# Kernel optimization log

Hardware: AMD Instinct MI355X
Metric: run time of the kernel (lower is better)

## Reference

```python
import jax, jax.numpy as jnp
import numpy as np

MAX_LENGTH = 10
SOS = 0


def setup_inputs() -> dict:
    key = jax.random.key(0)
    ks = jax.random.split(key, 16)
    B, S, H, V = 64, 128, 1024, 32000
    sc = 0.02
    return {
        "encoder_outputs": jax.random.normal(ks[0], (B, S, H), jnp.float32),
        "encoder_hidden": jax.random.normal(ks[1], (1, B, H), jnp.float32),
        "target_tensor": jax.random.randint(ks[2], (B, MAX_LENGTH), 0, V),
        "embedding": jax.random.normal(ks[3], (V, H), jnp.float32) * sc,
        "Wa_w": jax.random.normal(ks[4], (H, H), jnp.float32) * sc,
        "Wa_b": jnp.zeros((H,), jnp.float32),
        "Ua_w": jax.random.normal(ks[5], (H, H), jnp.float32) * sc,
        "Ua_b": jnp.zeros((H,), jnp.float32),
        "Va_w": jax.random.normal(ks[6], (1, H), jnp.float32) * sc,
        "Va_b": jnp.zeros((1,), jnp.float32),
        "gru_wi": jax.random.normal(ks[7], (3 * H, 2 * H), jnp.float32) * sc,
        "gru_wh": jax.random.normal(ks[8], (3 * H, H), jnp.float32) * sc,
        "gru_bi": jnp.zeros((3 * H,), jnp.float32),
        "gru_bh": jnp.zeros((3 * H,), jnp.float32),
        "out_w": jax.random.normal(ks[9], (V, H), jnp.float32) * sc,
        "out_b": jnp.zeros((V,), jnp.float32),
    }


def reference(encoder_outputs, encoder_hidden, target_tensor, embedding,
              Wa_w, Wa_b, Ua_w, Ua_b, Va_w, Va_b,
              gru_wi, gru_wh, gru_bi, gru_bh, out_w, out_b):
    B, S, H = encoder_outputs.shape
    # teacher-forced input tokens: [SOS, tgt_0, ..., tgt_{T-2}]
    tokens = jnp.concatenate(
        [jnp.full((B, 1), SOS, dtype=target_tensor.dtype),
         target_tensor[:, :MAX_LENGTH - 1]], axis=1)  # [B, T]
    emb_seq = embedding[tokens]                         # [B, T, H] (dropout = identity)
    # precompute Ua(keys), shared across steps
    Ua_keys = jnp.einsum('bsh,kh->bsk', encoder_outputs, Ua_w) + Ua_b  # [B,S,H]
    va = Va_w[0]

    def step(h, emb_t):  # h: [B,H], emb_t: [B,H]
        q = h @ Wa_w.T + Wa_b                                   # [B,H]
        scores = jnp.einsum('bsh,h->bs', jnp.tanh(q[:, None, :] + Ua_keys), va) + Va_b[0]
        w = jax.nn.softmax(scores, axis=-1)                     # [B,S]
        ctx = jnp.einsum('bs,bsh->bh', w, encoder_outputs)      # [B,H]
        x = jnp.concatenate([emb_t, ctx], axis=-1)              # [B,2H]
        gi = x @ gru_wi.T + gru_bi                              # [B,3H]
        gh = h @ gru_wh.T + gru_bh
        r = jax.nn.sigmoid(gi[:, :H] + gh[:, :H])
        z = jax.nn.sigmoid(gi[:, H:2 * H] + gh[:, H:2 * H])
        n = jnp.tanh(gi[:, 2 * H:] + r * gh[:, 2 * H:])
        h_new = (1.0 - z) * n + z * h
        return h_new, (h_new, w)

    h0 = encoder_hidden[0]  # [B,H]
    h_final, (outs, attns) = jax.lax.scan(step, h0, jnp.swapaxes(emb_seq, 0, 1))
    outs = jnp.swapaxes(outs, 0, 1)                 # [B,T,H]
    attns = jnp.swapaxes(attns, 0, 1)               # [B,T,S]
    logits = jnp.einsum('bth,vh->btv', outs, out_w) + out_b
    log_probs = jax.nn.log_softmax(logits, axis=-1)  # [B,T,V]
    return log_probs, h_final[None], attns
```

## Files before the change

kernel.cpp:

```cpp
#include <hip/hip_runtime.h>
#include <hip/hip_bf16.h>
#include <cstddef>

#define B 64
#define S 128
#define H 1024
#define V 32000
#define T 10
#define H3 3072
#define NCHUNK 250
#define SK_NB 256

typedef __bf16 bf16x8 __attribute__((ext_vector_type(8)));
typedef float f32x4 __attribute__((ext_vector_type(4)));
typedef unsigned short ushort8v __attribute__((ext_vector_type(8)));

__device__ inline unsigned short f2b(float f) {
    __hip_bfloat16 h = __float2bfloat16(f);
    return *reinterpret_cast<unsigned short*>(&h);
}
__device__ inline float b2f(unsigned short u) {
    return __uint_as_float(((unsigned)u) << 16);
}
__device__ inline float fast_tanh(float x) {
    float e = __expf(2.f * x);
    return 1.f - 2.f * __builtin_amdgcn_rcpf(e + 1.f);
}
__device__ inline float fast_sigmoid(float x) {
    return __builtin_amdgcn_rcpf(1.f + __expf(-x));
}
__device__ inline float2 sysload_f2(const float* p) {
    unsigned long long v = __hip_atomic_load((const unsigned long long*)p,
                                             __ATOMIC_RELAXED, __HIP_MEMORY_SCOPE_SYSTEM);
    float2 r;
    r.x = __uint_as_float((unsigned)v);
    r.y = __uint_as_float((unsigned)(v >> 32));
    return r;
}
__device__ inline void sysstore_f(float* p, float v) {
    __hip_atomic_store((unsigned*)p, __float_as_uint(v),
                       __ATOMIC_RELAXED, __HIP_MEMORY_SCOPE_SYSTEM);
}

__device__ inline int xcd_swz(int orig, int nwg) {
    int q = nwg >> 3, r = nwg & 7;
    int xcd = orig & 7, idx = orig >> 3;
    int base = (xcd < r) ? xcd * (q + 1) : r * (q + 1) + (xcd - r) * q;
    return base + idx;
}

#define PREP_NB 20240
__global__ void prep_kernel(const float* __restrict__ enc, unsigned short* __restrict__ enc_bf,
                            const float* __restrict__ Ua_w, unsigned short* __restrict__ Ua_bf,
                            const float* __restrict__ gwh, const float* __restrict__ Wa_w,
                            unsigned short* __restrict__ Wcat,
                            const float* __restrict__ gwi,
                            unsigned short* __restrict__ Wemb, unsigned short* __restrict__ Wctx,
                            const float* __restrict__ gbh, const float* __restrict__ Wa_b,
                            float* __restrict__ catbias,
                            const float* __restrict__ emb, const int* __restrict__ tgt,
                            unsigned short* __restrict__ embg,
                            const float* __restrict__ h0, unsigned short* __restrict__ hbf,
                            float* __restrict__ hbuf) {
    const int bid = blockIdx.x, tid = threadIdx.x;
    if (bid < 8192) {
        int i = bid * 256 + tid;
        float4 v = reinterpret_cast<const float4*>(enc)[i];
        ushort4 o = { f2b(v.x), f2b(v.y), f2b(v.z), f2b(v.w) };
        reinterpret_cast<ushort4*>(enc_bf)[i] = o;
    } else if (bid < 9216) {
        int i = (bid - 8192) * 256 + tid;
        float4 v = reinterpret_cast<const float4*>(Ua_w)[i];
        ushort4 o = { f2b(v.x), f2b(v.y), f2b(v.z), f2b(v.w) };
        reinterpret_cast<ushort4*>(Ua_bf)[i] = o;
    } else if (bid < 13312) {
        int i = (bid - 9216) * 256 + tid;
        int e = i * 4, n = e >> 10, k = e & 1023;
        const float* src = (n < H3) ? (gwh + (size_t)n * H + k) : (Wa_w + (size_t)(n - H3) * H + k);
        float4 v = *reinterpret_cast<const float4*>(src);
        ushort4 o = { f2b(v.x), f2b(v.y), f2b(v.z), f2b(v.w) };
        reinterpret_cast<ushort4*>(Wcat)[i] = o;
    } else if (bid < 16384) {
        int i = (bid - 13312) * 256 + tid;
        int e = i * 4, n = e >> 10, k = e & 1023;
        float4 v = *reinterpret_cast<const float4*>(gwi + (size_t)n * 2 * H + k);
        ushort4 o = { f2b(v.x), f2b(v.y), f2b(v.z), f2b(v.w) };
        reinterpret_cast<ushort4*>(Wemb)[i] = o;
    } else if (bid < 19456) {
        int i = (bid - 16384) * 256 + tid;
        int e = i * 4, n = e >> 10, k = e & 1023;
        float4 v = *reinterpret_cast<const float4*>(gwi + (size_t)n * 2 * H + H + k);
        ushort4 o = { f2b(v.x), f2b(v.y), f2b(v.z), f2b(v.w) };
        reinterpret_cast<ushort4*>(Wctx)[i] = o;
    } else if (bid < 19472) {
        int n = (bid - 19456) * 256 + tid;
        catbias[n] = (n < H3) ? gbh[n] : Wa_b[n - H3];
    } else if (bid < 20112) {
        int i = (bid - 19472) * 256 + tid;
        int e = i * 4;
        int t = e >> 16, rem = e & 65535;
        int b = rem >> 10, j = rem & 1023;
        int tok = (t == 0) ? 0 : tgt[b * T + (t - 1)];
        float4 v = *reinterpret_cast<const float4*>(emb + (size_t)tok * H + j);
        ushort4 o = { f2b(v.x), f2b(v.y), f2b(v.z), f2b(v.w) };
        *reinterpret_cast<ushort4*>(embg + ((size_t)t * B + b) * H + j) = o;
    } else if (bid < 20176) {
        int i = (bid - 20112) * 256 + tid;
        float4 v = reinterpret_cast<const float4*>(h0)[i];
        ushort4 o = { f2b(v.x), f2b(v.y), f2b(v.z), f2b(v.w) };
        reinterpret_cast<ushort4*>(hbf)[i] = o;
    } else {
        int i = (bid - 20176) * 256 + tid;
        reinterpret_cast<float4*>(hbuf)[i] = reinterpret_cast<const float4*>(h0)[i];
    }
}

struct GemmDesc {
    const unsigned short* A;
    const unsigned short* Bw;
    const float* bias;
    void* C;
    int M, N, out_bf16;
};

__global__ __launch_bounds__(512) void gemm3_kernel(GemmDesc d0, GemmDesc d1, GemmDesc d2,
                                                    const float* __restrict__ out_w,
                                                    unsigned short* __restrict__ outw_bf) {
    __shared__ unsigned short As[128][72];
    __shared__ unsigned short Bs[128][72];
    const int bid = blockIdx.x;
    const int tid = threadIdx.x;
    if (bid >= 2168) {
        int i = (bid - 2168) * 512 + tid;
        float4 v = reinterpret_cast<const float4*>(out_w)[i];
        ushort4 o = { f2b(v.x), f2b(v.y), f2b(v.z), f2b(v.w) };
        reinterpret_cast<ushort4*>(outw_bf)[i] = o;
        return;
    }
    GemmDesc d; int local, nwg;
    if (bid < 512)       { d = d0; local = bid;        nwg = 512;  }
    else if (bid < 2048) { d = d1; local = bid - 512;  nwg = 1536; }
    else                 { d = d2; local = bid - 2048; nwg = 120;  }
    local = xcd_swz(local, nwg);
    const int mtiles = d.M >> 7;
    const int bm = (local % mtiles) << 7, bn = (local / mtiles) << 7;
    const int lane = tid & 63, w = tid >> 6;
    const int wm = w >> 2, wn = w & 3;
    const int quad = lane >> 4, fr = lane & 15;
    f32x4 acc[4][2] = {};

    const int srow = tid >> 2, sc16 = (tid & 3) * 16;
    for (int k0 = 0; k0 < H; k0 += 64) {
        const unsigned short* ap = d.A + (size_t)(bm + srow) * H + k0 + sc16;
        *reinterpret_cast<bf16x8*>(&As[srow][sc16])     = *reinterpret_cast<const bf16x8*>(ap);
        *reinterpret_cast<bf16x8*>(&As[srow][sc16 + 8]) = *reinterpret_cast<const bf16x8*>(ap + 8);
        const unsigned short* bp = d.Bw + (size_t)(bn + srow) * H + k0 + sc16;
        *reinterpret_cast<bf16x8*>(&Bs[srow][sc16])     = *reinterpret_cast<const bf16x8*>(bp);
        *reinterpret_cast<bf16x8*>(&Bs[srow][sc16 + 8]) = *reinterpret_cast<const bf16x8*>(bp + 8);
        __syncthreads();
        #pragma unroll
        for (int ks = 0; ks < 2; ++ks) {
            const int kg = quad * 8 + 32 * ks;
            bf16x8 a[4], bb[2];
            #pragma unroll
            for (int m = 0; m < 4; ++m)
                a[m] = *reinterpret_cast<const bf16x8*>(&As[64 * wm + 16 * m + fr][kg]);
            #pragma unroll
            for (int n = 0; n < 2; ++n)
                bb[n] = *reinterpret_cast<const bf16x8*>(&Bs[32 * wn + 16 * n + fr][kg]);
            #pragma unroll
            for (int m = 0; m < 4; ++m)
                #pragma unroll
                for (int n = 0; n < 2; ++n)
                    acc[m][n] = __builtin_amdgcn_mfma_f32_16x16x32_bf16(a[m], bb[n], acc[m][n], 0, 0, 0);
        }
        __syncthreads();
    }
    #pragma unroll
    for (int n = 0; n < 2; ++n) {
        int col = bn + 32 * wn + 16 * n + fr;
        float bv = d.bias ? d.bias[col] : 0.f;
        #pragma unroll
        for (int m = 0; m < 4; ++m)
            #pragma unroll
            for (int i = 0; i < 4; ++i) {
                int row = bm + 64 * wm + 16 * m + quad * 4 + i;
                float v = acc[m][n][i] + bv;
                if (d.out_bf16)
                    ((unsigned short*)d.C)[(size_t)row * d.N + col] = f2b(v);
                else
                    ((float*)d.C)[(size_t)row * d.N + col] = v;
            }
    }
}

__global__ __launch_bounds__(512) void gemm_logits(const unsigned short* __restrict__ A,
                                                   const unsigned short* __restrict__ Bw,
                                                   const float* __restrict__ bias,
                                                   float* __restrict__ Cout,
                                                   float2* __restrict__ stats,
                                                   int M, int N, int K) {
    __shared__ unsigned short As[128][72];
    __shared__ unsigned short Bs[128][72];
    __shared__ float mred[128][4];
    __shared__ float sred[128][4];
    const int wg = xcd_swz(blockIdx.x, gridDim.x);
    const int mtiles = M >> 7;
    const int bm = (wg % mtiles) << 7, bn = (wg / mtiles) << 7;
    const int tid = threadIdx.x, lane = tid & 63, w = tid >> 6;
    const int wm = w >> 2, wn = w & 3;
    const int quad = lane >> 4, fr = lane & 15;
    f32x4 acc[4][2] = {};

    const int srow = tid >> 2, sc16 = (tid & 3) * 16;
    for (int k0 = 0; k0 < K; k0 += 64) {
        const unsigned short* ap = A + (size_t)(bm + srow) * K + k0 + sc16;
        *reinterpret_cast<bf16x8*>(&As[srow][sc16])     = *reinterpret_cast<const bf16x8*>(ap);
        *reinterpret_cast<bf16x8*>(&As[srow][sc16 + 8]) = *reinterpret_cast<const bf16x8*>(ap + 8);
        const unsigned short* bp = Bw + (size_t)(bn + srow) * K + k0 + sc16;
        *reinterpret_cast<bf16x8*>(&Bs[srow][sc16])     = *reinterpret_cast<const bf16x8*>(bp);
        *reinterpret_cast<bf16x8*>(&Bs[srow][sc16 + 8]) = *reinterpret_cast<const bf16x8*>(bp + 8);
        __syncthreads();
        #pragma unroll
        for (int ks = 0; ks < 2; ++ks) {
            const int kg = quad * 8 + 32 * ks;
            bf16x8 a[4], bb[2];
            #pragma unroll
            for (int m = 0; m < 4; ++m)
                a[m] = *reinterpret_cast<const bf16x8*>(&As[64 * wm + 16 * m + fr][kg]);
            #pragma unroll
            for (int n = 0; n < 2; ++n)
                bb[n] = *reinterpret_cast<const bf16x8*>(&Bs[32 * wn + 16 * n + fr][kg]);
            #pragma unroll
            for (int m = 0; m < 4; ++m)
                #pragma unroll
                for (int n = 0; n < 2; ++n)
                    acc[m][n] = __builtin_amdgcn_mfma_f32_16x16x32_bf16(a[m], bb[n], acc[m][n], 0, 0, 0);
        }
        __syncthreads();
    }

    #pragma unroll
    for (int n = 0; n < 2; ++n) {
        int col = bn + 32 * wn + 16 * n + fr;
        float bv = bias[col];
        #pragma unroll
        for (int m = 0; m < 4; ++m)
            #pragma unroll
            for (int i = 0; i < 4; ++i) {
                int row = bm + 64 * wm + 16 * m + quad * 4 + i;
                float v = acc[m][n][i] + bv;
                Cout[(size_t)row * N + col] = v;
                acc[m][n][i] = v;
            }
    }

    const int nchunk = N >> 7;
    #pragma unroll
    for (int m = 0; m < 4; ++m)
        #pragma unroll
        for (int i = 0; i < 4; ++i) {
            float x = fmaxf(acc[m][0][i], acc[m][1][i]);
            x = fmaxf(x, __shfl_xor(x, 1)); x = fmaxf(x, __shfl_xor(x, 2));
            x = fmaxf(x, __shfl_xor(x, 4)); x = fmaxf(x, __shfl_xor(x, 8));
            if (fr == 0) mred[64 * wm + 16 * m + quad * 4 + i][wn] = x;
        }
    __syncthreads();
    #pragma unroll
    for (int m = 0; m < 4; ++m)
        #pragma unroll
        for (int i = 0; i < 4; ++i) {
            int rl = 64 * wm + 16 * m + quad * 4 + i;
            float Mr = fmaxf(fmaxf(mred[rl][0], mred[rl][1]), fmaxf(mred[rl][2], mred[rl][3]));
            float sv = expf(acc[m][0][i] - Mr) + expf(acc[m][1][i] - Mr);
            sv += __shfl_xor(sv, 1); sv += __shfl_xor(sv, 2);
            sv += __shfl_xor(sv, 4); sv += __shfl_xor(sv, 8);
            if (fr == 0) sred[rl][wn] = sv;
        }
    __syncthreads();
    if (tid < 128) {
        float Mr = fmaxf(fmaxf(mred[tid][0], mred[tid][1]), fmaxf(mred[tid][2], mred[tid][3]));
        float Sv = sred[tid][0] + sred[tid][1] + sred[tid][2] + sred[tid][3];
        stats[(size_t)(bm + tid) * nchunk + (bn >> 7)] = make_float2(Mr, Sv);
    }
}

__global__ __launch_bounds__(256) void step_kernel(const unsigned short* __restrict__ hbf_in,
                                                   const unsigned short* __restrict__ Wcat,
                                                   const float* __restrict__ catbias,
                                                   float* __restrict__ ghq,
                                                   const unsigned short* __restrict__ keys,
                                                   const unsigned short* __restrict__ KV,
                                                   const float* __restrict__ va,
                                                   const float* __restrict__ va_b,
                                                   const float* __restrict__ gi_emb,
                                                   float* __restrict__ h,
                                                   unsigned short* __restrict__ hbf_out,
                                                   unsigned short* __restrict__ outs_bf,
                                                   float* __restrict__ attns,
                                                   float* __restrict__ h_final,
                                                   unsigned int* __restrict__ ctr, int t) {
    __shared__ unsigned short As[64][136];
    __shared__ unsigned short Bsm[16][136];
    __shared__ float ssc[128];
    __shared__ float sw[128];
    __shared__ float red[4][64][13];
    const int bid = blockIdx.x;
    const int tid = threadIdx.x, lane = tid & 63, wv = tid >> 6;
    const int quad = lane >> 4, fr = lane & 15;

    {
        const int bn = bid * 16;
        f32x4 acc = {};
        const int srA = tid >> 2, scA = (tid & 3) * 32;
        const int srB = tid >> 4, scB = (tid & 15) * 8;
        for (int k0 = 0; k0 < H; k0 += 128) {
            const unsigned short* ap = hbf_in + (size_t)srA * H + k0 + scA;
            #pragma unroll
            for (int u = 0; u < 4; ++u)
                *reinterpret_cast<bf16x8*>(&As[srA][scA + 8 * u]) =
                    *reinterpret_cast<const bf16x8*>(ap + 8 * u);
            const unsigned short* bp = Wcat + (size_t)(bn + srB) * H + k0 + scB;
            *reinterpret_cast<bf16x8*>(&Bsm[srB][scB]) = *reinterpret_cast<const bf16x8*>(bp);
            __syncthreads();
            #pragma unroll
            for (int ks = 0; ks < 4; ++ks) {
                const int kg = quad * 8 + 32 * ks;
                bf16x8 a = *reinterpret_cast<const bf16x8*>(&As[16 * wv + fr][kg]);
                bf16x8 bb = *reinterpret_cast<const bf16x8*>(&Bsm[fr][kg]);
                acc = __builtin_amdgcn_mfma_f32_16x16x32_bf16(a, bb, acc, 0, 0, 0);
            }
            __syncthreads();
        }
        int col = bn + fr;
        float bv = catbias[col];
        #pragma unroll
        for (int i = 0; i < 4; ++i) {
            int row = 16 * wv + quad * 4 + i;
            sysstore_f(&ghq[(size_t)row * 4096 + col], acc[i] + bv);
        }
    }

    __syncthreads();
    if (tid == 0) {
        atomicAdd(ctr, 1u);
        while (__hip_atomic_load(ctr, __ATOMIC_RELAXED, __HIP_MEMORY_SCOPE_AGENT) < SK_NB)
            __builtin_amdgcn_s_sleep(1);
    }
    __syncthreads();
    asm volatile("" ::: "memory");

    const int q = bid & 3, b = bid >> 2;
    float qv[16], vv[16];
    {
        const float* qp = ghq + (size_t)b * 4096 + H3 + lane * 16;
        const float* vp = va + lane * 16;
        #pragma unroll
        for (int j = 0; j < 8; ++j) {
            float2 f = sysload_f2(qp + j * 2);
            qv[j * 2] = f.x; qv[j * 2 + 1] = f.y;
        }
        #pragma unroll
        for (int j = 0; j < 16; ++j) vv[j] = vp[j];
    }
    const float vab = va_b[0];
    const unsigned short* kb = keys + (size_t)b * S * H;
    for (int i = 0; i < 32; i += 2) {
        int s0 = wv * 32 + i;
        const unsigned short* kr0 = kb + (size_t)s0 * H + lane * 16;
        const unsigned short* kr1 = kr0 + H;
        ushort8v k00 = *reinterpret_cast<const ushort8v*>(kr0);
        ushort8v k01 = *reinterpret_cast<const ushort8v*>(kr0 + 8);
        ushort8v k10 = *reinterpret_cast<const ushort8v*>(kr1);
        ushort8v k11 = *reinterpret_cast<const ushort8v*>(kr1 + 8);
        float a0 = 0.f, a1 = 0.f;
        #pragma unroll
        for (int e = 0; e < 8; ++e) {
            a0 += fast_tanh(qv[e] + b2f(k00[e])) * vv[e];
            a1 += fast_tanh(qv[e] + b2f(k10[e])) * vv[e];
        }
        #pragma unroll
        for (int e = 0; e < 8; ++e) {
            a0 += fast_tanh(qv[8 + e] + b2f(k01[e])) * vv[8 + e];
            a1 += fast_tanh(qv[8 + e] + b2f(k11[e])) * vv[8 + e];
        }
        a0 += __shfl_xor(a0, 1);  a1 += __shfl_xor(a1, 1);
        a0 += __shfl_xor(a0, 2);  a1 += __shfl_xor(a1, 2);
        a0 += __shfl_xor(a0, 4);  a1 += __shfl_xor(a1, 4);
        a0 += __shfl_xor(a0, 8);  a1 += __shfl_xor(a1, 8);
        a0 += __shfl_xor(a0, 16); a1 += __shfl_xor(a1, 16);
        a0 += __shfl_xor(a0, 32); a1 += __shfl_xor(a1, 32);
        if (lane == 0) { ssc[s0] = a0 + vab; ssc[s0 + 1] = a1 + vab; }
    }
    __syncthreads();
    if (tid < 128) {
        float mx = -1e30f;
        #pragma unroll 8
        for (int s = 0; s < 128; ++s) mx = fmaxf(mx, ssc[s]);
        float sum = 0.f;
        #pragma unroll 8
        for (int s = 0; s < 128; ++s) sum += __expf(ssc[s] - mx);
        float wvv = __expf(ssc[tid] - mx) / sum;
        sw[tid] = wvv;
        if (q == 0) attns[((size_t)b * T + t) * S + tid] = wvv;
    }
    __syncthreads();

    const int j0 = q * 256 + lane * 4;
    float ar[4] = {}, az[4] = {}, an[4] = {};
    const unsigned short* kvb = KV + (size_t)b * S * H3 + j0;
    for (int i = 0; i < 32; i += 2) {
        int s0 = wv * 32 + i;
        float w0 = sw[s0], w1 = sw[s0 + 1];
        const unsigned short* r0 = kvb + (size_t)s0 * H3;
        const unsigned short* r1 = r0 + H3;
        uint2 u0a = *reinterpret_cast<const uint2*>(r0);
        uint2 u1a = *reinterpret_cast<const uint2*>(r0 + 1024);
        uint2 u2a = *reinterpret_cast<const uint2*>(r0 + 2048);
        uint2 u0b = *reinterpret_cast<const uint2*>(r1);
        uint2 u1b = *reinterpret_cast<const uint2*>(r1 + 1024);
        uint2 u2b = *reinterpret_cast<const uint2*>(r1 + 2048);
        ar[0] += w0 * b2f((unsigned short)(u0a.x & 0xffff)) + w1 * b2f((unsigned short)(u0b.x & 0xffff));
        ar[1] += w0 * b2f((unsigned short)(u0a.x >> 16))    + w1 * b2f((unsigned short)(u0b.x >> 16));
        ar[2] += w0 * b2f((unsigned short)(u0a.y & 0xffff)) + w1 * b2f((unsigned short)(u0b.y & 0xffff));
        ar[3] += w0 * b2f((unsigned short)(u0a.y >> 16))    + w1 * b2f((unsigned short)(u0b.y >> 16));
        az[0] += w0 * b2f((unsigned short)(u1a.x & 0xffff)) + w1 * b2f((unsigned short)(u1b.x & 0xffff));
        az[1] += w0 * b2f((unsigned short)(u1a.x >> 16))    + w1 * b2f((unsigned short)(u1b.x >> 16));
        az[2] += w0 * b2f((unsigned short)(u1a.y & 0xffff)) + w1 * b2f((unsigned short)(u1b.y & 0xffff));
        az[3] += w0 * b2f((unsigned short)(u1a.y >> 16))    + w1 * b2f((unsigned short)(u1b.y >> 16));
        an[0] += w0 * b2f((unsigned short)(u2a.x & 0xffff)) + w1 * b2f((unsigned short)(u2b.x & 0xffff));
        an[1] += w0 * b2f((unsigned short)(u2a.x >> 16))    + w1 * b2f((unsigned short)(u2b.x >> 16));
        an[2] += w0 * b2f((unsigned short)(u2a.y & 0xffff)) + w1 * b2f((unsigned short)(u2b.y & 0xffff));
        an[3] += w0 * b2f((unsigned short)(u2a.y >> 16))    + w1 * b2f((unsigned short)(u2b.y >> 16));
    }
    #pragma unroll
    for (int g = 0; g < 4; ++g) {
        red[wv][lane][g]     = ar[g];
        red[wv][lane][4 + g] = az[g];
        red[wv][lane][8 + g] = an[g];
    }
    __syncthreads();

    if (tid < 64) {
        float rr[4], zz[4], nn[4];
        #pragma unroll
        for (int g = 0; g < 4; ++g) {
            rr[g] = red[0][tid][g] + red[1][tid][g] + red[2][tid][g] + red[3][tid][g];
            zz[g] = red[0][tid][4+g] + red[1][tid][4+g] + red[2][tid][4+g] + red[3][tid][4+g];
            nn[g] = red[0][tid][8+g] + red[1][tid][8+g] + red[2][tid][8+g] + red[3][tid][8+g];
        }
        const int jj = q * 256 + tid * 4;
        const float* ge = gi_emb + ((size_t)t * B + b) * H3;
        const float* gh = ghq + (size_t)b * 4096;
        float geR[4], geZ[4], geN[4], ghR[4], ghZ[4], ghN[4], hv[4];
        *reinterpret_cast<float4*>(geR) = *reinterpret_cast<const float4*>(ge + jj);
        *reinterpret_cast<float4*>(geZ) = *reinterpret_cast<const float4*>(ge + 1024 + jj);
        *reinterpret_cast<float4*>(geN) = *reinterpret_cast<const float4*>(ge + 2048 + jj);
        float2 f;
        f = sysload_f2(gh + jj);            ghR[0] = f.x; ghR[1] = f.y;
        f = sysload_f2(gh + jj + 2);        ghR[2] = f.x; ghR[3] = f.y;
        f = sysload_f2(gh + 1024 + jj);     ghZ[0] = f.x; ghZ[1] = f.y;
        f = sysload_f2(gh + 1024 + jj + 2); ghZ[2] = f.x; ghZ[3] = f.y;
        f = sysload_f2(gh + 2048 + jj);     ghN[0] = f.x; ghN[1] = f.y;
        f = sysload_f2(gh + 2048 + jj + 2); ghN[2] = f.x; ghN[3] = f.y;
        *reinterpret_cast<float4*>(hv) = *reinterpret_cast<const float4*>(h + (size_t)b * H + jj);
        ushort4 hb;
        unsigned short* hbp = reinterpret_cast<unsigned short*>(&hb);
        #pragma unroll
        for (int i = 0; i < 4; ++i) {
            float r = fast_sigmoid(geR[i] + rr[i] + ghR[i]);
            float z = fast_sigmoid(geZ[i] + zz[i] + ghZ[i]);
            float n = fast_tanh(geN[i] + nn[i] + r * ghN[i]);
            hv[i] = (1.f - z) * n + z * hv[i];
            hbp[i] = f2b(hv[i]);
        }
        *reinterpret_cast<float4*>(h + (size_t)b * H + jj) = *reinterpret_cast<float4*>(hv);
        *reinterpret_cast<ushort4*>(hbf_out + (size_t)b * H + jj) = hb;
        *reinterpret_cast<ushort4*>(outs_bf + ((size_t)b * T + t) * H + jj) = hb;
        if (t == T - 1)
            *reinterpret_cast<float4*>(h_final + (size_t)b * H + jj) = *reinterpret_cast<float4*>(hv);
    }
}

__global__ void lsesub_kernel(const float2* __restrict__ stats, float* __restrict__ x) {
    const int row = blockIdx.x;
    const int tid = threadIdx.x;
    __shared__ float shm[256];
    __shared__ float shs[256];
    float mv = -1e30f, sv = 0.f;
    float2 st = make_float2(-1e30f, 0.f);
    if (tid < NCHUNK) { st = stats[(size_t)row * NCHUNK + tid]; mv = st.x; }
    shm[tid] = mv; __syncthreads();
    for (int off = 128; off > 0; off >>= 1) {
        if (tid < off) shm[tid] = fmaxf(shm[tid], shm[tid + off]);
        __syncthreads();
    }
    float M = shm[0]; __syncthreads();
    if (tid < NCHUNK) sv = st.y * expf(st.x - M);
    shs[tid] = sv; __syncthreads();
    for (int off = 128; off > 0; off >>= 1) {
        if (tid < off) shs[tid] += shs[tid + off];
        __syncthreads();
    }
    float L = M + logf(shs[0]);
    __syncthreads();
    float4* p = reinterpret_cast<float4*>(x + (size_t)row * V);
    for (int i = tid; i < V / 4; i += 256) {
        float4 v = p[i];
        v.x -= L; v.y -= L; v.z -= L; v.w -= L;
        p[i] = v;
    }
}


extern "C" void kernel_launch(void* const* d_in, const int* in_sizes, int n_in,
                              void* d_out, int out_size, void* d_ws, size_t ws_size,
                              hipStream_t stream) {
    const float* enc   = (const float*)d_in[0];
    const float* h0    = (const float*)d_in[1];
    const int*   tgt   = (const int*)d_in[2];
    const float* emb   = (const float*)d_in[3];
    const float* Wa_w  = (const float*)d_in[4];
    const float* Wa_b  = (const float*)d_in[5];
    const float* Ua_w  = (const float*)d_in[6];
    const float* Ua_b  = (const float*)d_in[7];
    const float* Va_w  = (const float*)d_in[8];
    const float* Va_b  = (const float*)d_in[9];
    const float* gwi   = (const float*)d_in[10];
    const float* gwh   = (const float*)d_in[11];
    const float* gbi   = (const float*)d_in[12];
    const float* gbh   = (const float*)d_in[13];
    const float* out_w = (const float*)d_in[14];
    const float* out_b = (const float*)d_in[15];

    float* out       = (float*)d_out;
    float* log_probs = out;
    float* h_final   = out + (size_t)B * T * V;
    float* attns     = h_final + (size_t)B * H;

    char* pp = (char*)d_ws;
    auto alloc = [&](size_t bytes) { char* r = pp; pp += (bytes + 255) & ~(size_t)255; return r; };
    unsigned short* ua_bf   = (unsigned short*)alloc((size_t)B * S * H * 2);
    unsigned short* enc_bf  = (unsigned short*)alloc((size_t)B * S * H * 2);
    unsigned short* outw_bf = (unsigned short*)alloc((size_t)V * H * 2);
    unsigned short* KV      = (unsigned short*)alloc((size_t)B * S * H3 * 2);
    unsigned short* Ua_bf   = (unsigned short*)alloc((size_t)H * H * 2);
    unsigned short* Wcat    = (unsigned short*)alloc((size_t)4096 * H * 2);
    unsigned short* Wctx    = (unsigned short*)alloc((size_t)H3 * H * 2);
    unsigned short* Wemb    = (unsigned short*)alloc((size_t)H3 * H * 2);
    float*          catbias = (float*)alloc(4096 * 4);
    unsigned short* embg    = (unsigned short*)alloc((size_t)T * B * H * 2);
    float*          gi_emb  = (float*)alloc((size_t)T * B * H3 * 4);
    float*          hbuf    = (float*)alloc((size_t)B * H * 4);
    unsigned short* hbf     = (unsigned short*)alloc((size_t)B * H * 2);
    float*          ghq     = (float*)alloc((size_t)B * 4096 * 4);
    unsigned short* outs_bf = (unsigned short*)alloc((size_t)B * T * H * 2);
    float2*         stats   = (float2*)alloc((size_t)B * T * NCHUNK * 8);
    unsigned int*   ctrs    = (unsigned int*)alloc(T * 4);

    hipMemsetAsync(ctrs, 0, T * sizeof(unsigned int), stream);

    prep_kernel<<<PREP_NB, 256, 0, stream>>>(enc, enc_bf, Ua_w, Ua_bf,
                                             gwh, Wa_w, Wcat, gwi, Wemb, Wctx,
                                             gbh, Wa_b, catbias, emb, tgt, embg,
                                             h0, hbf, hbuf);

    GemmDesc d0 = { enc_bf, Ua_bf, Ua_b, (void*)ua_bf,  B * S, H,  1 };
    GemmDesc d1 = { enc_bf, Wctx,  nullptr, (void*)KV,  B * S, H3, 1 };
    GemmDesc d2 = { embg,   Wemb,  gbi, (void*)gi_emb,  T * B, H3, 0 };
    gemm3_kernel<<<18168, 512, 0, stream>>>(d0, d1, d2, out_w, outw_bf);

    for (int t = 0; t < T; ++t) {
        step_kernel<<<SK_NB, 256, 0, stream>>>(hbf, Wcat, catbias, ghq, ua_bf, KV,
                                               Va_w, Va_b, gi_emb, hbuf, hbf, outs_bf,
                                               attns, h_final, ctrs + t, t);
    }

    gemm_logits<<<(B * T / 128) * (V / 128), 512, 0, stream>>>(
        outs_bf, outw_bf, out_b, log_probs, stats, B * T, V, H);
    lsesub_kernel<<<B * T, 256, 0, stream>>>(stats, log_probs);
}
```

Baseline: 734.7 us.

## Use direct global-to-LDS loads in GEMMs, register-direct step GEMM, hierarchical barrier

The two tiled GEMM kernels now stage A/B tiles with global_load_lds (16-byte direct-to-LDS loads) using an unpadded 32-wide K tile. This removes the VGPR round trip and halves LDS per tile, but also halves the K step, so each tile needs twice as many barriers. The step kernel's small h·Wcat GEMM drops LDS staging and feeds MFMA fragments straight from global memory. Its grid-wide spin barrier becomes a two-level counter (8 groups of 32 blocks on separate cache lines) to reduce atomic contention. The unpadded LDS layout may cause bank conflicts on the fragment reads.

```diff
diff --git a/kernel.cpp b/kernel.cpp
--- a/kernel.cpp
+++ b/kernel.cpp
@@ -29,6 +29,13 @@
 __device__ inline float fast_sigmoid(float x) {
     return __builtin_amdgcn_rcpf(1.f + __expf(-x));
 }
+
+__device__ inline void gload_lds16(const void* g, void* l) {
+    __builtin_amdgcn_global_load_lds(
+        (const __attribute__((address_space(1))) void*)g,
+        (__attribute__((address_space(3))) void*)l, 16, 0, 0);
+}
+
 __device__ inline float2 sysload_f2(const float* p) {
     unsigned long long v = __hip_atomic_load((const unsigned long long*)p,
                                              __ATOMIC_RELAXED, __HIP_MEMORY_SCOPE_SYSTEM);
@@ -126,8 +133,8 @@
 __global__ __launch_bounds__(512) void gemm3_kernel(GemmDesc d0, GemmDesc d1, GemmDesc d2,
                                                     const float* __restrict__ out_w,
                                                     unsigned short* __restrict__ outw_bf) {
-    __shared__ unsigned short As[128][72];
-    __shared__ unsigned short Bs[128][72];
+    __shared__ unsigned short As[128 * 32];
+    __shared__ unsigned short Bs[128 * 32];
     const int bid = blockIdx.x;
     const int tid = threadIdx.x;
     if (bid >= 2168) {
@@ -147,33 +154,32 @@
     const int lane = tid & 63, w = tid >> 6;
     const int wm = w >> 2, wn = w & 3;
     const int quad = lane >> 4, fr = lane & 15;
+    const int K = H;
     f32x4 acc[4][2] = {};
 
-    const int srow = tid >> 2, sc16 = (tid & 3) * 16;
-    for (int k0 = 0; k0 < H; k0 += 64) {
-        const unsigned short* ap = d.A + (size_t)(bm + srow) * H + k0 + sc16;
-        *reinterpret_cast<bf16x8*>(&As[srow][sc16])     = *reinterpret_cast<const bf16x8*>(ap);
-        *reinterpret_cast<bf16x8*>(&As[srow][sc16 + 8]) = *reinterpret_cast<const bf16x8*>(ap + 8);
-        const unsigned short* bp = d.Bw + (size_t)(bn + srow) * H + k0 + sc16;
-        *reinterpret_cast<bf16x8*>(&Bs[srow][sc16])     = *reinterpret_cast<const bf16x8*>(bp);
-        *reinterpret_cast<bf16x8*>(&Bs[srow][sc16 + 8]) = *reinterpret_cast<const bf16x8*>(bp + 8);
+    const int sr = w * 16 + (lane >> 2), sc = (lane & 3) * 8;
+    const unsigned short* agp = d.A + (size_t)(bm + sr) * K + sc;
+    const unsigned short* bgp = d.Bw + (size_t)(bn + sr) * K + sc;
+    unsigned short* alp = As + w * 512;
+    unsigned short* blp = Bs + w * 512;
+
+    for (int k0 = 0; k0 < K; k0 += 32) {
+        gload_lds16(agp + k0, alp);
+        gload_lds16(bgp + k0, blp);
         __syncthreads();
-        #pragma unroll
-        for (int ks = 0; ks < 2; ++ks) {
-            const int kg = quad * 8 + 32 * ks;
-            bf16x8 a[4], bb[2];
-            #pragma unroll
-            for (int m = 0; m < 4; ++m)
-                a[m] = *reinterpret_cast<const bf16x8*>(&As[64 * wm + 16 * m + fr][kg]);
+        const int kg = quad * 8;
+        bf16x8 a[4], bb[2];
+        #pragma unroll
+        for (int m = 0; m < 4; ++m)
+            a[m] = *reinterpret_cast<const bf16x8*>(&As[(64 * wm + 16 * m + fr) * 32 + kg]);
+        #pragma unroll
+        for (int n = 0; n < 2; ++n)
+            bb[n] = *reinterpret_cast<const bf16x8*>(&Bs[(32 * wn + 16 * n + fr) * 32 + kg]);
+        #pragma unroll
+        for (int m = 0; m < 4; ++m)
             #pragma unroll
             for (int n = 0; n < 2; ++n)
-                bb[n] = *reinterpret_cast<const bf16x8*>(&Bs[32 * wn + 16 * n + fr][kg]);
-            #pragma unroll
-            for (int m = 0; m < 4; ++m)
-                #pragma unroll
-                for (int n = 0; n < 2; ++n)
-                    acc[m][n] = __builtin_amdgcn_mfma_f32_16x16x32_bf16(a[m], bb[n], acc[m][n], 0, 0, 0);
-        }
+                acc[m][n] = __builtin_amdgcn_mfma_f32_16x16x32_bf16(a[m], bb[n], acc[m][n], 0, 0, 0);
         __syncthreads();
     }
     #pragma unroll
@@ -200,8 +206,8 @@
                                                    float* __restrict__ Cout,
                                                    float2* __restrict__ stats,
                                                    int M, int N, int K) {
-    __shared__ unsigned short As[128][72];
-    __shared__ unsigned short Bs[128][72];
+    __shared__ unsigned short As[128 * 32];
+    __shared__ unsigned short Bs[128 * 32];
     __shared__ float mred[128][4];
     __shared__ float sred[128][4];
     const int wg = xcd_swz(blockIdx.x, gridDim.x);
@@ -212,31 +218,29 @@
     const int quad = lane >> 4, fr = lane & 15;
     f32x4 acc[4][2] = {};
 
-    const int srow = tid >> 2, sc16 = (tid & 3) * 16;
-    for (int k0 = 0; k0 < K; k0 += 64) {
-        const unsigned short* ap = A + (size_t)(bm + srow) * K + k0 + sc16;
-        *reinterpret_cast<bf16x8*>(&As[srow][sc16])     = *reinterpret_cast<const bf16x8*>(ap);
-        *reinterpret_cast<bf16x8*>(&As[srow][sc16 + 8]) = *reinterpret_cast<const bf16x8*>(ap + 8);
-        const unsigned short* bp = Bw + (size_t)(bn + srow) * K + k0 + sc16;
-        *reinterpret_cast<bf16x8*>(&Bs[srow][sc16])     = *reinterpret_cast<const bf16x8*>(bp);
-        *reinterpret_cast<bf16x8*>(&Bs[srow][sc16 + 8]) = *reinterpret_cast<const bf16x8*>(bp + 8);
+    const int sr = w * 16 + (lane >> 2), sc = (lane & 3) * 8;
+    const unsigned short* agp = A + (size_t)(bm + sr) * K + sc;
+    const unsigned short* bgp = Bw + (size_t)(bn + sr) * K + sc;
+    unsigned short* alp = As + w * 512;
+    unsigned short* blp = Bs + w * 512;
+
+    for (int k0 = 0; k0 < K; k0 += 32) {
+        gload_lds16(agp + k0, alp);
+        gload_lds16(bgp + k0, blp);
         __syncthreads();
-        #pragma unroll
-        for (int ks = 0; ks < 2; ++ks) {
-            const int kg = quad * 8 + 32 * ks;
-            bf16x8 a[4], bb[2];
-            #pragma unroll
-            for (int m = 0; m < 4; ++m)
-                a[m] = *reinterpret_cast<const bf16x8*>(&As[64 * wm + 16 * m + fr][kg]);
+        const int kg = quad * 8;
+        bf16x8 a[4], bb[2];
+        #pragma unroll
+        for (int m = 0; m < 4; ++m)
+            a[m] = *reinterpret_cast<const bf16x8*>(&As[(64 * wm + 16 * m + fr) * 32 + kg]);
+        #pragma unroll
+        for (int n = 0; n < 2; ++n)
+            bb[n] = *reinterpret_cast<const bf16x8*>(&Bs[(32 * wn + 16 * n + fr) * 32 + kg]);
+        #pragma unroll
+        for (int m = 0; m < 4; ++m)
             #pragma unroll
             for (int n = 0; n < 2; ++n)
-                bb[n] = *reinterpret_cast<const bf16x8*>(&Bs[32 * wn + 16 * n + fr][kg]);
-            #pragma unroll
-            for (int m = 0; m < 4; ++m)
-                #pragma unroll
-                for (int n = 0; n < 2; ++n)
-                    acc[m][n] = __builtin_amdgcn_mfma_f32_16x16x32_bf16(a[m], bb[n], acc[m][n], 0, 0, 0);
-        }
+                acc[m][n] = __builtin_amdgcn_mfma_f32_16x16x32_bf16(a[m], bb[n], acc[m][n], 0, 0, 0);
         __syncthreads();
     }
 
@@ -300,8 +304,6 @@
                                                    float* __restrict__ attns,
                                                    float* __restrict__ h_final,
                                                    unsigned int* __restrict__ ctr, int t) {
-    __shared__ unsigned short As[64][136];
-    __shared__ unsigned short Bsm[16][136];
     __shared__ float ssc[128];
     __shared__ float sw[128];
     __shared__ float red[4][64][13];
@@ -312,25 +314,13 @@
     {
         const int bn = bid * 16;
         f32x4 acc = {};
-        const int srA = tid >> 2, scA = (tid & 3) * 32;
-        const int srB = tid >> 4, scB = (tid & 15) * 8;
-        for (int k0 = 0; k0 < H; k0 += 128) {
-            const unsigned short* ap = hbf_in + (size_t)srA * H + k0 + scA;
-            #pragma unroll
-            for (int u = 0; u < 4; ++u)
-                *reinterpret_cast<bf16x8*>(&As[srA][scA + 8 * u]) =
-                    *reinterpret_cast<const bf16x8*>(ap + 8 * u);
-            const unsigned short* bp = Wcat + (size_t)(bn + srB) * H + k0 + scB;
-            *reinterpret_cast<bf16x8*>(&Bsm[srB][scB]) = *reinterpret_cast<const bf16x8*>(bp);
-            __syncthreads();
-            #pragma unroll
-            for (int ks = 0; ks < 4; ++ks) {
-                const int kg = quad * 8 + 32 * ks;
-                bf16x8 a = *reinterpret_cast<const bf16x8*>(&As[16 * wv + fr][kg]);
-                bf16x8 bb = *reinterpret_cast<const bf16x8*>(&Bsm[fr][kg]);
-                acc = __builtin_amdgcn_mfma_f32_16x16x32_bf16(a, bb, acc, 0, 0, 0);
-            }
-            __syncthreads();
+        const unsigned short* ap = hbf_in + (size_t)(16 * wv + fr) * H + quad * 8;
+        const unsigned short* bp = Wcat + (size_t)(bn + fr) * H + quad * 8;
+        #pragma unroll
+        for (int k0 = 0; k0 < H; k0 += 32) {
+            bf16x8 a = *reinterpret_cast<const bf16x8*>(ap + k0);
+            bf16x8 bb = *reinterpret_cast<const bf16x8*>(bp + k0);
+            acc = __builtin_amdgcn_mfma_f32_16x16x32_bf16(a, bb, acc, 0, 0, 0);
         }
         int col = bn + fr;
         float bv = catbias[col];
@@ -343,9 +333,10 @@
 
     __syncthreads();
     if (tid == 0) {
-        atomicAdd(ctr, 1u);
-        while (__hip_atomic_load(ctr, __ATOMIC_RELAXED, __HIP_MEMORY_SCOPE_AGENT) < SK_NB)
-            __builtin_amdgcn_s_sleep(1);
+        unsigned old = atomicAdd(&ctr[(1 + (bid >> 5)) * 32], 1u);
+        if (old == 31u) atomicAdd(&ctr[0], 1u);
+        while (__hip_atomic_load(&ctr[0], __ATOMIC_RELAXED, __HIP_MEMORY_SCOPE_AGENT) < 8u)
+            __builtin_amdgcn_s_sleep(2);
     }
     __syncthreads();
     asm volatile("" ::: "memory");
@@ -556,9 +547,9 @@
     float*          ghq     = (float*)alloc((size_t)B * 4096 * 4);
     unsigned short* outs_bf = (unsigned short*)alloc((size_t)B * T * H * 2);
     float2*         stats   = (float2*)alloc((size_t)B * T * NCHUNK * 8);
-    unsigned int*   ctrs    = (unsigned int*)alloc(T * 4);
-
-    hipMemsetAsync(ctrs, 0, T * sizeof(unsigned int), stream);
+    unsigned int*   ctrs    = (unsigned int*)alloc((size_t)T * 9 * 32 * 4);
+
+    hipMemsetAsync(ctrs, 0, (size_t)T * 9 * 32 * 4, stream);
 
     prep_kernel<<<PREP_NB, 256, 0, stream>>>(enc, enc_bf, Ua_w, Ua_bf,
                                              gwh, Wa_w, Wcat, gwi, Wemb, Wctx,
@@ -573,7 +564,7 @@
     for (int t = 0; t < T; ++t) {
         step_kernel<<<SK_NB, 256, 0, stream>>>(hbf, Wcat, catbias, ghq, ua_bf, KV,
                                                Va_w, Va_b, gi_emb, hbuf, hbf, outs_bf,
-                                               attns, h_final, ctrs + t, t);
+                                               attns, h_final, ctrs + (size_t)t * 9 * 32, t);
     }
 
     gemm_logits<<<(B * T / 128) * (V / 128), 512, 0, stream>>>(
```

Measured after the change: 730.3 us. No clear change (-0.6%).
